# Optimization experiments

Hardware: AMD Instinct MI355X
Metric: run time of the kernel (lower is better)

The kernel has to match this reference:

```python
import jax, jax.numpy as jnp
import numpy as np

D_MODEL = 1024
HEADS = 16
HEAD_DIM = D_MODEL // HEADS
SEQ_LEN = 2048
BATCH = 2
LN_EPS = 1e-5


def _layernorm(x, gamma, beta):
    mu = jnp.mean(x, axis=-1, keepdims=True)
    var = jnp.var(x, axis=-1, keepdims=True)
    return (x - mu) * jax.lax.rsqrt(var + LN_EPS) * gamma + beta


def setup_inputs() -> dict:
    key = jax.random.key(0)
    ks = jax.random.split(key, 12)
    d, h = D_MODEL, 4 * D_MODEL
    s = lambda fan_in: 1.0 / np.sqrt(fan_in)
    return {
        "x": jax.random.normal(ks[0], (BATCH, SEQ_LEN, d), dtype=jnp.float32),
        "W_qkv": jax.random.uniform(ks[1], (d, 3 * d), minval=-s(d), maxval=s(d)),
        "b_qkv": jax.random.uniform(ks[2], (3 * d,), minval=-s(d), maxval=s(d)),
        "W1": jax.random.uniform(ks[3], (d, h), minval=-s(d), maxval=s(d)),
        "b1": jax.random.uniform(ks[4], (h,), minval=-s(d), maxval=s(d)),
        "W2": jax.random.uniform(ks[5], (h, d), minval=-s(h), maxval=s(h)),
        "b2": jax.random.uniform(ks[6], (d,), minval=-s(h), maxval=s(h)),
        "ln1_g": jnp.ones((d,), jnp.float32),
        "ln1_b": jnp.zeros((d,), jnp.float32),
        "ln2_g": jnp.ones((d,), jnp.float32),
        "ln2_b": jnp.zeros((d,), jnp.float32),
    }


def reference(x, W_qkv, b_qkv, W1, b1, W2, b2, ln1_g, ln1_b, ln2_g, ln2_b):
    B, T, C = x.shape
    # QKV projection -> [B, T, 3, H, hs] -> q,k,v each [B, H, T, hs]
    qkv = (x @ W_qkv + b_qkv).reshape(B, T, 3, HEADS, HEAD_DIM)
    qkv = jnp.transpose(qkv, (2, 0, 3, 1, 4))
    q, k, v = qkv[0], qkv[1], qkv[2]
    # Naive causal attention with full [B,H,T,T] score matrix (matches source)
    A = jnp.einsum("bhqd,bhkd->bhqk", q, k) / jnp.sqrt(jnp.float32(HEAD_DIM))
    causal = jnp.tril(jnp.ones((T, T), dtype=bool))
    A = jnp.where(causal, A, -jnp.inf)
    A = jax.nn.softmax(A, axis=-1)
    attn = jnp.einsum("bhqk,bhkd->bhqd", A, v)  # [B,H,T,hs]
    attn = jnp.transpose(attn, (0, 2, 1, 3)).reshape(B, T, C)
    # Residual + LN, FFN, residual + LN (dropout=0 / eval)
    h = _layernorm(x + attn, ln1_g, ln1_b)
    ff = jax.nn.relu(h @ W1 + b1) @ W2 + b2
    return _layernorm(h + ff, ln2_g, ln2_b)
```

## Files before the change

kernel.cpp:

```cpp
#include <hip/hip_runtime.h>

#define D_MODEL 1024
#define HEADS   16
#define HEAD_DIM 64
#define SEQ     2048
#define BATCH   2
#define ROWS    (BATCH*SEQ)
#define FFDIM   4096

typedef __attribute__((ext_vector_type(8))) short short8;
typedef __attribute__((ext_vector_type(4))) float f32x4;
typedef __attribute__((ext_vector_type(4))) unsigned short us4;

typedef const __attribute__((address_space(1))) unsigned int* gptr_t;
typedef __attribute__((address_space(3))) unsigned int* lptr_t;

__device__ __forceinline__ unsigned short f2bf(float f){
  unsigned int x = __float_as_uint(f);
  x += 0x7fffu + ((x >> 16) & 1u);
  return (unsigned short)(x >> 16);
}

__device__ __forceinline__ float wave_sum(float x){
  #pragma unroll
  for (int off = 32; off; off >>= 1) x += __shfl_xor(x, off);
  return x;
}

__global__ __launch_bounds__(256) void cast_bf16_kernel(const float* __restrict__ in,
                                                        unsigned short* __restrict__ out, int n4){
  int i = blockIdx.x * 256 + threadIdx.x;
  if (i >= n4) return;
  float4 v = *(const float4*)(in + (size_t)i * 4);
  us4 o;
  o[0] = f2bf(v.x); o[1] = f2bf(v.y); o[2] = f2bf(v.z); o[3] = f2bf(v.w);
  *(us4*)(out + (size_t)i * 4) = o;
}

__global__ __launch_bounds__(256) void transpose_cast_kernel(const float* __restrict__ in,
                                                             unsigned short* __restrict__ out,
                                                             int R, int C){
  __shared__ float tile[32][33];
  const int bc = blockIdx.x * 32, br = blockIdx.y * 32;
  const int tx = threadIdx.x & 31, ty = threadIdx.x >> 5;
  #pragma unroll
  for (int j = 0; j < 4; ++j)
    tile[ty + 8*j][tx] = in[(size_t)(br + ty + 8*j) * C + bc + tx];
  __syncthreads();
  #pragma unroll
  for (int j = 0; j < 4; ++j)
    out[(size_t)(bc + ty + 8*j) * R + br + tx] = f2bf(tile[tx][ty + 8*j]);
}

template<int EPI>
__global__ __launch_bounds__(512, 1) void gemm8p_kernel(const unsigned short* __restrict__ A,
                                                        const unsigned short* __restrict__ BT,
                                                        const float* __restrict__ bias,
                                                        int M, int N, int K, int kchunk,
                                                        int gx, int gy,
                                                        unsigned short* __restrict__ outH,
                                                        unsigned short* __restrict__ qo,
                                                        unsigned short* __restrict__ ko,
                                                        unsigned short* __restrict__ vT){
  __shared__ __align__(16) unsigned short Ab[2][2][256 * 32];
  __shared__ __align__(16) unsigned short Bb[2][2][256 * 32];
  const int tid = threadIdx.x, lane = tid & 63, wid = tid >> 6;
  const int wm = wid >> 2, wn = wid & 3;
  const int lr = lane & 15, g = lane >> 4;

  const int nwg = gridDim.x, cpx = nwg >> 3;
  const int wg = (blockIdx.x & 7) * cpx + (blockIdx.x >> 3);
  const int nx = wg % gx;
  const int rest = wg / gx;
  const int my = rest % gy;
  const int sk = rest / gy;
  const int m0 = my * 256, n0 = nx * 256, kb0 = sk * kchunk;
  const int nk = kchunk >> 6;

  f32x4 acc[8][4];
  #pragma unroll
  for (int i = 0; i < 8; ++i)
    #pragma unroll
    for (int j = 0; j < 4; ++j)
      acc[i][j] = f32x4{0.f, 0.f, 0.f, 0.f};

  auto STAGE = [&](int op, int t, int kh){
    const int d = t & 1;
    unsigned short* base = op ? &Bb[d][kh][0] : &Ab[d][kh][0];
    const unsigned short* src = op ? BT : A;
    const int r0 = op ? n0 : m0;
    #pragma unroll
    for (int j = 0; j < 2; ++j){
      const int L = tid + j * 512;
      const int row = L >> 2, c = L & 3;
      __builtin_amdgcn_global_load_lds(
          (gptr_t)(const void*)(src + (size_t)(r0 + row) * K + kb0 + t * 64 + kh * 32
                                + ((c ^ ((row >> 1) & 3)) << 3)),
          (lptr_t)(void*)(base + L * 8), 16, 0, 0);
    }
  };

  STAGE(0,0,0); STAGE(1,0,0); STAGE(0,0,1); STAGE(1,0,1);
  STAGE(0,1,0); STAGE(1,1,0); STAGE(0,1,1); STAGE(1,1,1);
  asm volatile("s_waitcnt vmcnt(8)" ::: "memory");
  __builtin_amdgcn_s_barrier();

  short8 afr[8], bfr[4];

  #define PHASE_SYNC(T)                                              \
    if ((T) < 2)              asm volatile("s_waitcnt vmcnt(4)" ::: "memory"); \
    else if ((T) <= nk - 3)   asm volatile("s_waitcnt vmcnt(8)" ::: "memory"); \
    else                      asm volatile("s_waitcnt vmcnt(0)" ::: "memory"); \
    __builtin_amdgcn_s_barrier();                                    \
    asm volatile("s_waitcnt lgkmcnt(0)" ::: "memory");               \
    __builtin_amdgcn_sched_barrier(0);

  for (int t = 0; t < nk; ++t){
    const int d = t & 1;
    #pragma unroll
    for (int i = 0; i < 8; ++i){
      const int row = wm * 128 + i * 16 + lr;
      afr[i] = *(const short8*)&Ab[d][0][row * 32 + ((g ^ ((row >> 1) & 3)) << 3)];
    }
    #pragma unroll
    for (int j = 0; j < 2; ++j){
      const int row = wn * 64 + j * 16 + lr;
      bfr[j] = *(const short8*)&Bb[d][0][row * 32 + ((g ^ ((row >> 1) & 3)) << 3)];
    }
    if (t >= 1 && t + 1 < nk) STAGE(1, t + 1, 1);
    PHASE_SYNC(t)
    __builtin_amdgcn_s_setprio(1);
    #pragma unroll
    for (int i = 0; i < 8; ++i){
      acc[i][0] = __builtin_amdgcn_mfma_f32_16x16x32_bf16(afr[i], bfr[0], acc[i][0], 0, 0, 0);
      acc[i][1] = __builtin_amdgcn_mfma_f32_16x16x32_bf16(afr[i], bfr[1], acc[i][1], 0, 0, 0);
    }
    __builtin_amdgcn_s_setprio(0);
    __builtin_amdgcn_s_barrier();

    #pragma unroll
    for (int j = 0; j < 2; ++j){
      const int row = wn * 64 + (2 + j) * 16 + lr;
      bfr[2 + j] = *(const short8*)&Bb[d][0][row * 32 + ((g ^ ((row >> 1) & 3)) << 3)];
    }
    if (t + 2 < nk) STAGE(0, t + 2, 0);
    PHASE_SYNC(t)
    __builtin_amdgcn_s_setprio(1);
    #pragma unroll
    for (int i = 0; i < 8; ++i){
      acc[i][2] = __builtin_amdgcn_mfma_f32_16x16x32_bf16(afr[i], bfr[2], acc[i][2], 0, 0, 0);
      acc[i][3] = __builtin_amdgcn_mfma_f32_16x16x32_bf16(afr[i], bfr[3], acc[i][3], 0, 0, 0);
    }
    __builtin_amdgcn_s_setprio(0);
    __builtin_amdgcn_s_barrier();

    #pragma unroll
    for (int i = 0; i < 8; ++i){
      const int row = wm * 128 + i * 16 + lr;
      afr[i] = *(const short8*)&Ab[d][1][row * 32 + ((g ^ ((row >> 1) & 3)) << 3)];
    }
    #pragma unroll
    for (int j = 0; j < 2; ++j){
      const int row = wn * 64 + j * 16 + lr;
      bfr[j] = *(const short8*)&Bb[d][1][row * 32 + ((g ^ ((row >> 1) & 3)) << 3)];
    }
    if (t + 2 < nk) STAGE(1, t + 2, 0);
    PHASE_SYNC(t)
    __builtin_amdgcn_s_setprio(1);
    #pragma unroll
    for (int i = 0; i < 8; ++i){
      acc[i][0] = __builtin_amdgcn_mfma_f32_16x16x32_bf16(afr[i], bfr[0], acc[i][0], 0, 0, 0);
      acc[i][1] = __builtin_amdgcn_mfma_f32_16x16x32_bf16(afr[i], bfr[1], acc[i][1], 0, 0, 0);
    }
    __builtin_amdgcn_s_setprio(0);
    __builtin_amdgcn_s_barrier();

    #pragma unroll
    for (int j = 0; j < 2; ++j){
      const int row = wn * 64 + (2 + j) * 16 + lr;
      bfr[2 + j] = *(const short8*)&Bb[d][1][row * 32 + ((g ^ ((row >> 1) & 3)) << 3)];
    }
    if (t + 2 < nk) STAGE(0, t + 2, 1);
    PHASE_SYNC(t)
    __builtin_amdgcn_s_setprio(1);
    #pragma unroll
    for (int i = 0; i < 8; ++i){
      acc[i][2] = __builtin_amdgcn_mfma_f32_16x16x32_bf16(afr[i], bfr[2], acc[i][2], 0, 0, 0);
      acc[i][3] = __builtin_amdgcn_mfma_f32_16x16x32_bf16(afr[i], bfr[3], acc[i][3], 0, 0, 0);
    }
    __builtin_amdgcn_s_setprio(0);
    __builtin_amdgcn_s_barrier();
  }
  #undef PHASE_SYNC

  #pragma unroll
  for (int i = 0; i < 8; ++i){
    const int rg = m0 + wm * 128 + i * 16 + g * 4;
    #pragma unroll
    for (int j = 0; j < 4; ++j){
      const int cg = n0 + wn * 64 + j * 16 + lr;
      if constexpr (EPI == 0){
        const float bb = bias[cg];
        const int which = cg >> 10, rem = cg & 1023;
        const int hh = rem >> 6, dd = rem & 63;
        const int bb_ = rg >> 11, tt = rg & 2047;
        const size_t bh = (size_t)(bb_ * HEADS + hh);
        if (which == 2){
          us4 pk;
          #pragma unroll
          for (int r = 0; r < 4; ++r) pk[r] = f2bf(acc[i][j][r] + bb);
          *(us4*)(vT + (bh * 64 + dd) * SEQ + tt) = pk;
        } else {
          unsigned short* dst = which ? ko : qo;
          const float sc2 = which ? 1.0f : 0.18033688f;
          #pragma unroll
          for (int r = 0; r < 4; ++r)
            dst[(bh * SEQ + tt + r) * 64 + dd] = f2bf((acc[i][j][r] + bb) * sc2);
        }
      } else if constexpr (EPI == 1){
        const float bb = bias[cg];
        #pragma unroll
        for (int r = 0; r < 4; ++r)
          outH[(size_t)(rg + r) * N + cg] = f2bf(fmaxf(acc[i][j][r] + bb, 0.f));
      } else {
        unsigned short* dst = outH + (size_t)sk * M * N;
        #pragma unroll
        for (int r = 0; r < 4; ++r)
          dst[(size_t)(rg + r) * N + cg] = f2bf(acc[i][j][r]);
      }
    }
  }
}

template<int EPI>
__global__ __launch_bounds__(256) void gemm_kernel(const unsigned short* __restrict__ A,
                                                   const unsigned short* __restrict__ BT,
                                                   const float* __restrict__ bias,
                                                   int M, int N, int K, int kchunk,
                                                   int gx, int gy,
                                                   float* __restrict__ outF,
                                                   unsigned short* __restrict__ outH){
  __shared__ __align__(16) unsigned short Alds[2][128 * 32];
  __shared__ __align__(16) unsigned short Blds[2][128 * 32];
  const int tid = threadIdx.x;
  const int lane = tid & 63;
  const int wid = tid >> 6;
  const int wr = wid >> 1, wc = wid & 1;
  const int lrow = lane & 15, lgrp = lane >> 4;

  const int nwg = gridDim.x;
  const int cpx = nwg >> 3;
  const int wg = (blockIdx.x & 7) * cpx + (blockIdx.x >> 3);
  const int nx = wg % gx;
  const int rest = wg / gx;
  const int my = rest % gy;
  const int sk = rest / gy;

  const int m0 = my * 128, n0 = nx * 128;
  const int kbase0 = sk * kchunk;
  const int sr = lane >> 2, sc = (lane & 3) * 8;

  f32x4 acc[4][4];
  #pragma unroll
  for (int i = 0; i < 4; ++i)
    #pragma unroll
    for (int j = 0; j < 4; ++j)
      acc[i][j] = f32x4{0.f, 0.f, 0.f, 0.f};

  #pragma unroll
  for (int it = 0; it < 2; ++it){
    const int c = wid * 2 + it;
    const int r = c * 16 + sr;
    __builtin_amdgcn_global_load_lds(
        (gptr_t)(const void*)(A + (size_t)(m0 + r) * K + kbase0 + sc),
        (lptr_t)(void*)(&Alds[0][c * 512]), 16, 0, 0);
    __builtin_amdgcn_global_load_lds(
        (gptr_t)(const void*)(BT + (size_t)(n0 + r) * K + kbase0 + sc),
        (lptr_t)(void*)(&Blds[0][c * 512]), 16, 0, 0);
  }

  const int nk = kchunk >> 5;
  int cur = 0;
  for (int kt = 0; kt < nk; ++kt){
    __syncthreads();
    if (kt + 1 < nk){
      const int kb = kbase0 + (kt + 1) * 32;
      #pragma unroll
      for (int it = 0; it < 2; ++it){
        const int c = wid * 2 + it;
        const int r = c * 16 + sr;
        __builtin_amdgcn_global_load_lds(
            (gptr_t)(const void*)(A + (size_t)(m0 + r) * K + kb + sc),
            (lptr_t)(void*)(&Alds[cur ^ 1][c * 512]), 16, 0, 0);
        __builtin_amdgcn_global_load_lds(
            (gptr_t)(const void*)(BT + (size_t)(n0 + r) * K + kb + sc),
            (lptr_t)(void*)(&Blds[cur ^ 1][c * 512]), 16, 0, 0);
      }
    }
    short8 af[4], bfr[4];
    #pragma unroll
    for (int f = 0; f < 4; ++f){
      af[f]  = *(const short8*)&Alds[cur][(wr * 64 + f * 16 + lrow) * 32 + lgrp * 8];
      bfr[f] = *(const short8*)&Blds[cur][(wc * 64 + f * 16 + lrow) * 32 + lgrp * 8];
    }
    #pragma unroll
    for (int i = 0; i < 4; ++i)
      #pragma unroll
      for (int j = 0; j < 4; ++j)
        acc[i][j] = __builtin_amdgcn_mfma_f32_16x16x32_bf16(af[i], bfr[j], acc[i][j], 0, 0, 0);
    cur ^= 1;
  }

  float* const outP = outF + (size_t)sk * M * N;
  #pragma unroll
  for (int i = 0; i < 4; ++i){
    const int rg = m0 + wr * 64 + i * 16 + lgrp * 4;
    #pragma unroll
    for (int j = 0; j < 4; ++j){
      const int cg = n0 + wc * 64 + j * 16 + lrow;
      #pragma unroll
      for (int r = 0; r < 4; ++r)
        outP[(size_t)(rg + r) * N + cg] = acc[i][j][r];
    }
  }
  (void)bias; (void)outH;
}

__global__ __launch_bounds__(256) void attn_mfma_kernel(const unsigned short* __restrict__ Qb,
                                                        const unsigned short* __restrict__ Kb,
                                                        const unsigned short* __restrict__ VT,
                                                        float* __restrict__ Op){
  __shared__ __align__(16) char Kl[2][8192];
  __shared__ __align__(16) char Vl[2][8192];
  __shared__ __align__(16) char Pl[4][4096];
  const int tid = threadIdx.x;
  const int w = tid >> 6, lane = tid & 63;
  const int lr = lane & 15, g = lane >> 4;

  const int bx = blockIdx.x, u = bx & 255, half = bx >> 8;
  const int g8 = u >> 5;
  const int qg = half ? g8 : 15 - g8;
  const int bh = u & 31;

  const int q0w = qg * 128 + w * 32;
  const int qA = q0w + lr, qB = qA + 16;

  const char* const KbB = (const char*)(Kb + (size_t)bh * SEQ * 64);
  const char* const VbB = (const char*)(VT + (size_t)bh * 64 * SEQ);
  char* const PbA = Pl[w];
  char* const PbB = Pl[w] + 2048;

  const unsigned short* qra = Qb + ((size_t)bh * SEQ + qA) * 64 + g * 8;
  const short8 qfA0 = *(const short8*)(qra);
  const short8 qfA1 = *(const short8*)(qra + 32);
  const short8 qfB0 = *(const short8*)(qra + 16 * 64);
  const short8 qfB1 = *(const short8*)(qra + 16 * 64 + 32);

  f32x4 oA[4], oB[4];
  #pragma unroll
  for (int dt = 0; dt < 4; ++dt){ oA[dt] = f32x4{0.f,0.f,0.f,0.f}; oB[dt] = f32x4{0.f,0.f,0.f,0.f}; }
  float lA = 0.f, lB = 0.f;
  const int swzl = (lr & 7) << 4;

  const int kbmax = 2 * qg + 1;

  short8 st[4];
  {
    #pragma unroll
    for (int c = 0; c < 2; ++c){
      const int L = c * 4096 + tid * 16;
      st[c] = *(const short8*)(KbB + L);
      const int row = L >> 7, col = L & 127;
      st[2 + c] = *(const short8*)(VbB + (size_t)row * 4096 + col);
    }
  }

  for (int kb = 0; kb <= kbmax; ++kb){
    const int p = kb & 1;
    const int k0 = kb * 64;

    #pragma unroll
    for (int c = 0; c < 2; ++c){
      const int L = c * 4096 + tid * 16;
      const int row = L >> 7, col = L & 127;
      const int dst = row * 128 + (col ^ ((row & 7) << 4));
      *(short8*)(Kl[p] + dst) = st[c];
      *(short8*)(Vl[p] + dst) = st[2 + c];
    }
    __syncthreads();

    if (kb < kbmax){
      #pragma unroll
      for (int c = 0; c < 2; ++c){
        const int L = c * 4096 + tid * 16;
        st[c] = *(const short8*)(KbB + (size_t)(kb + 1) * 8192 + L);
        const int row = L >> 7, col = L & 127;
        st[2 + c] = *(const short8*)(VbB + (size_t)row * 4096 + (size_t)(kb + 1) * 128 + col);
      }
    }

    f32x4 sA[4], sB[4];
    __builtin_amdgcn_s_setprio(1);
    #pragma unroll
    for (int kt = 0; kt < 4; ++kt){
      const int row = kt * 16 + lr;
      const int ro = row * 128, sw = (row & 7) << 4;
      const short8 kf0 = *(const short8*)(Kl[p] + ro + ((g * 16) ^ sw));
      const short8 kf1 = *(const short8*)(Kl[p] + ro + ((64 + g * 16) ^ sw));
      sA[kt] = __builtin_amdgcn_mfma_f32_16x16x32_bf16(kf0, qfA0, f32x4{0.f,0.f,0.f,0.f}, 0, 0, 0);
      sA[kt] = __builtin_amdgcn_mfma_f32_16x16x32_bf16(kf1, qfA1, sA[kt], 0, 0, 0);
      sB[kt] = __builtin_amdgcn_mfma_f32_16x16x32_bf16(kf0, qfB0, f32x4{0.f,0.f,0.f,0.f}, 0, 0, 0);
      sB[kt] = __builtin_amdgcn_mfma_f32_16x16x32_bf16(kf1, qfB1, sB[kt], 0, 0, 0);
    }
    __builtin_amdgcn_s_setprio(0);

    if (kb >= kbmax - 1){
      #pragma unroll
      for (int kt = 0; kt < 4; ++kt)
        #pragma unroll
        for (int r = 0; r < 4; ++r){
          const int key = k0 + kt * 16 + g * 4 + r;
          if (key > qA) sA[kt][r] = -INFINITY;
          if (key > qB) sB[kt][r] = -INFINITY;
        }
    }

    {
      float sum = 0.f;
      #pragma unroll
      for (int kt = 0; kt < 4; ++kt){
        #pragma unroll
        for (int r = 0; r < 4; ++r){
          const float pp = __builtin_amdgcn_exp2f(sA[kt][r]);
          sA[kt][r] = pp; sum += pp;
        }
        unsigned int p01, p23;
        asm("v_cvt_pk_bf16_f32 %0, %1, %2" : "=v"(p01) : "v"(sA[kt][0]), "v"(sA[kt][1]));
        asm("v_cvt_pk_bf16_f32 %0, %1, %2" : "=v"(p23) : "v"(sA[kt][2]), "v"(sA[kt][3]));
        uint2 pk; pk.x = p01; pk.y = p23;
        *(uint2*)(PbA + lr * 128 + ((kt * 32 + g * 8) ^ swzl)) = pk;
      }
      sum += __shfl_xor(sum, 16);
      sum += __shfl_xor(sum, 32);
      lA += sum;
    }
    {
      float sum = 0.f;
      #pragma unroll
      for (int kt = 0; kt < 4; ++kt){
        #pragma unroll
        for (int r = 0; r < 4; ++r){
          const float pp = __builtin_amdgcn_exp2f(sB[kt][r]);
          sB[kt][r] = pp; sum += pp;
        }
        unsigned int p01, p23;
        asm("v_cvt_pk_bf16_f32 %0, %1, %2" : "=v"(p01) : "v"(sB[kt][0]), "v"(sB[kt][1]));
        asm("v_cvt_pk_bf16_f32 %0, %1, %2" : "=v"(p23) : "v"(sB[kt][2]), "v"(sB[kt][3]));
        uint2 pk; pk.x = p01; pk.y = p23;
        *(uint2*)(PbB + lr * 128 + ((kt * 32 + g * 8) ^ swzl)) = pk;
      }
      sum += __shfl_xor(sum, 16);
      sum += __shfl_xor(sum, 32);
      lB += sum;
    }

    const short8 paA0 = *(const short8*)(PbA + lr * 128 + ((g * 16) ^ swzl));
    const short8 paA1 = *(const short8*)(PbA + lr * 128 + ((64 + g * 16) ^ swzl));
    const short8 paB0 = *(const short8*)(PbB + lr * 128 + ((g * 16) ^ swzl));
    const short8 paB1 = *(const short8*)(PbB + lr * 128 + ((64 + g * 16) ^ swzl));
    __builtin_amdgcn_s_setprio(1);
    #pragma unroll
    for (int dt = 0; dt < 4; ++dt){
      const int row = dt * 16 + lr;
      const int ro = row * 128, sw = (row & 7) << 4;
      const short8 vf0 = *(const short8*)(Vl[p] + ro + ((g * 16) ^ sw));
      const short8 vf1 = *(const short8*)(Vl[p] + ro + ((64 + g * 16) ^ sw));
      oA[dt] = __builtin_amdgcn_mfma_f32_16x16x32_bf16(paA0, vf0, oA[dt], 0, 0, 0);
      oA[dt] = __builtin_amdgcn_mfma_f32_16x16x32_bf16(paA1, vf1, oA[dt], 0, 0, 0);
      oB[dt] = __builtin_amdgcn_mfma_f32_16x16x32_bf16(paB0, vf0, oB[dt], 0, 0, 0);
      oB[dt] = __builtin_amdgcn_mfma_f32_16x16x32_bf16(paB1, vf1, oB[dt], 0, 0, 0);
    }
    __builtin_amdgcn_s_setprio(0);
  }

  const int b = bh >> 4, hh = bh & 15;
  {
    float lv[4];
    #pragma unroll
    for (int r = 0; r < 4; ++r) lv[r] = __shfl(lA, g * 4 + r);
    #pragma unroll
    for (int dt = 0; dt < 4; ++dt)
      #pragma unroll
      for (int r = 0; r < 4; ++r)
        Op[((size_t)(b * SEQ) + q0w + g * 4 + r) * D_MODEL + hh * 64 + dt * 16 + lr] = oA[dt][r] / lv[r];
  }
  {
    float lv[4];
    #pragma unroll
    for (int r = 0; r < 4; ++r) lv[r] = __shfl(lB, g * 4 + r);
    #pragma unroll
    for (int dt = 0; dt < 4; ++dt)
      #pragma unroll
      for (int r = 0; r < 4; ++r)
        Op[((size_t)(b * SEQ) + q0w + 16 + g * 4 + r) * D_MODEL + hh * 64 + dt * 16 + lr] = oB[dt][r] / lv[r];
  }
}

__global__ __launch_bounds__(256) void ln_kernel(const float* __restrict__ A,
                                                 const float* __restrict__ B1,
                                                 const unsigned short* __restrict__ P4,
                                                 size_t pstride,
                                                 const float* __restrict__ bias,
                                                 const float* __restrict__ g,
                                                 const float* __restrict__ be,
                                                 float* __restrict__ outF,
                                                 unsigned short* __restrict__ outH){
  const int row = blockIdx.x, tid = threadIdx.x;
  const size_t base = (size_t)row * D_MODEL + tid * 4;
  float4 va = *(const float4*)(A + base);
  float v0 = va.x, v1 = va.y, v2 = va.z, v3 = va.w;
  if (B1){
    float4 vb = *(const float4*)(B1 + base);
    v0 += vb.x; v1 += vb.y; v2 += vb.z; v3 += vb.w;
  }
  if (P4){
    #pragma unroll
    for (int p = 0; p < 4; ++p){
      us4 u = *(const us4*)(P4 + p * pstride + base);
      v0 += __uint_as_float((unsigned int)u[0] << 16);
      v1 += __uint_as_float((unsigned int)u[1] << 16);
      v2 += __uint_as_float((unsigned int)u[2] << 16);
      v3 += __uint_as_float((unsigned int)u[3] << 16);
    }
  }
  if (bias){
    float4 vd = *(const float4*)(bias + tid * 4);
    v0 += vd.x; v1 += vd.y; v2 += vd.z; v3 += vd.w;
  }
  float s  = v0 + v1 + v2 + v3;
  float ss = v0*v0 + v1*v1 + v2*v2 + v3*v3;
  s = wave_sum(s); ss = wave_sum(ss);
  __shared__ float red[8];
  const int w = tid >> 6, lane = tid & 63;
  if (!lane){ red[w] = s; red[4 + w] = ss; }
  __syncthreads();
  s  = red[0] + red[1] + red[2] + red[3];
  ss = red[4] + red[5] + red[6] + red[7];
  const float mu  = s * (1.0f / D_MODEL);
  const float var = ss * (1.0f / D_MODEL) - mu * mu;
  const float rstd = rsqrtf(var + 1e-5f);
  float4 gg = *(const float4*)(g  + tid * 4);
  float4 bb = *(const float4*)(be + tid * 4);
  const float r0 = (v0 - mu) * rstd * gg.x + bb.x;
  const float r1 = (v1 - mu) * rstd * gg.y + bb.y;
  const float r2 = (v2 - mu) * rstd * gg.z + bb.z;
  const float r3 = (v3 - mu) * rstd * gg.w + bb.w;
  float4 of; of.x = r0; of.y = r1; of.z = r2; of.w = r3;
  *(float4*)(outF + base) = of;
  if (outH){
    us4 oh; oh[0] = f2bf(r0); oh[1] = f2bf(r1); oh[2] = f2bf(r2); oh[3] = f2bf(r3);
    *(us4*)(outH + base) = oh;
  }
}

__global__ __launch_bounds__(256) void ln2f_kernel(const float* __restrict__ A,
                                                   const float* __restrict__ B1,
                                                   const float* __restrict__ bias,
                                                   const float* __restrict__ g,
                                                   const float* __restrict__ be,
                                                   float* __restrict__ outF){
  const int row = blockIdx.x, tid = threadIdx.x;
  const size_t base = (size_t)row * D_MODEL + tid * 4;
  float4 va = *(const float4*)(A + base);
  float4 vb = *(const float4*)(B1 + base);
  float4 vd = *(const float4*)(bias + tid * 4);
  float v0 = va.x + vb.x + vd.x, v1 = va.y + vb.y + vd.y;
  float v2 = va.z + vb.z + vd.z, v3 = va.w + vb.w + vd.w;
  float s  = v0 + v1 + v2 + v3;
  float ss = v0*v0 + v1*v1 + v2*v2 + v3*v3;
  s = wave_sum(s); ss = wave_sum(ss);
  __shared__ float red[8];
  const int w = tid >> 6, lane = tid & 63;
  if (!lane){ red[w] = s; red[4 + w] = ss; }
  __syncthreads();
  s  = red[0] + red[1] + red[2] + red[3];
  ss = red[4] + red[5] + red[6] + red[7];
  const float mu  = s * (1.0f / D_MODEL);
  const float var = ss * (1.0f / D_MODEL) - mu * mu;
  const float rstd = rsqrtf(var + 1e-5f);
  float4 gg = *(const float4*)(g  + tid * 4);
  float4 bb = *(const float4*)(be + tid * 4);
  float4 of;
  of.x = (v0 - mu) * rstd * gg.x + bb.x;
  of.y = (v1 - mu) * rstd * gg.y + bb.y;
  of.z = (v2 - mu) * rstd * gg.z + bb.z;
  of.w = (v3 - mu) * rstd * gg.w + bb.w;
  *(float4*)(outF + base) = of;
}

extern "C" void kernel_launch(void* const* d_in, const int* in_sizes, int n_in,
                              void* d_out, int out_size, void* d_ws, size_t ws_size,
                              hipStream_t stream){
  (void)in_sizes; (void)n_in; (void)out_size;
  const float* x     = (const float*)d_in[0];
  const float* W_qkv = (const float*)d_in[1];
  const float* b_qkv = (const float*)d_in[2];
  const float* W1    = (const float*)d_in[3];
  const float* b1    = (const float*)d_in[4];
  const float* W2    = (const float*)d_in[5];
  const float* b2    = (const float*)d_in[6];
  const float* ln1g  = (const float*)d_in[7];
  const float* ln1b  = (const float*)d_in[8];
  const float* ln2g  = (const float*)d_in[9];
  const float* ln2b  = (const float*)d_in[10];

  char* ws = (char*)d_ws;
  const size_t MB = 1024ull * 1024ull;
  unsigned short* WqkvT = (unsigned short*)(ws + 0 * MB);
  unsigned short* W1T   = (unsigned short*)(ws + 6 * MB);
  unsigned short* W2T   = (unsigned short*)(ws + 14 * MB);
  unsigned short* xbf   = (unsigned short*)(ws + 22 * MB);
  unsigned short* qB    = (unsigned short*)(ws + 30 * MB);
  unsigned short* kB    = (unsigned short*)(ws + 39 * MB);
  unsigned short* vT    = (unsigned short*)(ws + 48 * MB);
  float* attn = (float*)(ws + 57 * MB);
  float* hF           = (float*)(ws + 30 * MB);
  unsigned short* hB  = (unsigned short*)(ws + 46 * MB);
  unsigned short* ff1 = (unsigned short*)(ws + 54 * MB);
  unsigned short* pbf = (unsigned short*)(ws + 86 * MB);
  float* p0           = (float*)(ws + 86 * MB);

  const int use8p = (ws_size >= 118 * MB);

  cast_bf16_kernel<<<4096, 256, 0, stream>>>(x, xbf, ROWS * D_MODEL / 4);
  transpose_cast_kernel<<<dim3(96, 32), 256, 0, stream>>>(W_qkv, WqkvT, 1024, 3072);
  transpose_cast_kernel<<<dim3(128, 32), 256, 0, stream>>>(W1, W1T, 1024, 4096);
  transpose_cast_kernel<<<dim3(32, 128), 256, 0, stream>>>(W2, W2T, 4096, 1024);

  gemm8p_kernel<0><<<192, 512, 0, stream>>>(
      xbf, WqkvT, b_qkv, ROWS, 3072, 1024, 1024, 12, 16, nullptr, qB, kB, vT);

  attn_mfma_kernel<<<512, 256, 0, stream>>>(qB, kB, vT, attn);

  ln_kernel<<<ROWS, 256, 0, stream>>>(x, attn, nullptr, 0, nullptr, ln1g, ln1b, hF, hB);

  gemm8p_kernel<1><<<256, 512, 0, stream>>>(
      hB, W1T, b1, ROWS, FFDIM, 1024, 1024, 16, 16, ff1, nullptr, nullptr, nullptr);

  if (use8p){
    gemm8p_kernel<4><<<256, 512, 0, stream>>>(
        ff1, W2T, nullptr, ROWS, 1024, FFDIM, 1024, 4, 16, pbf, nullptr, nullptr, nullptr);
    ln_kernel<<<ROWS, 256, 0, stream>>>(hF, nullptr, pbf, (size_t)ROWS * 1024, b2,
                                        ln2g, ln2b, (float*)d_out, nullptr);
  } else {
    gemm_kernel<3><<<256, 256, 0, stream>>>(
        ff1, W2T, nullptr, ROWS, 1024, FFDIM, FFDIM, 8, 32, p0, nullptr);
    ln2f_kernel<<<ROWS, 256, 0, stream>>>(hF, p0, b2, ln2g, ln2b, (float*)d_out);
  }
}
```

Measured before the change: 206.2 us.

## Move QKV GEMM to 128-tile kernel and retune 8-phase vmcnt waits

The QKV projection now runs on the simpler 128x128 double-buffered GEMM with 768 workgroups instead of the 256x256 eight-phase kernel with 192 workgroups, which left most of the 256 CUs idle. The 8-phase kernel, still used for the FFN GEMMs, gets a different waitcnt scheme: the initial wait allows 12 loads in flight and waits happen only in two of the four phases, so more loads stay outstanding. The smaller-tile GEMM reuses less data per load and uses a simpler pipeline, and the looser waits need careful counting to stay correct.

```diff
diff --git a/kernel.cpp b/kernel.cpp
--- a/kernel.cpp
+++ b/kernel.cpp
@@ -53,152 +53,94 @@
 }
 
 template<int EPI>
-__global__ __launch_bounds__(512, 1) void gemm8p_kernel(const unsigned short* __restrict__ A,
-                                                        const unsigned short* __restrict__ BT,
-                                                        const float* __restrict__ bias,
-                                                        int M, int N, int K, int kchunk,
-                                                        int gx, int gy,
-                                                        unsigned short* __restrict__ outH,
-                                                        unsigned short* __restrict__ qo,
-                                                        unsigned short* __restrict__ ko,
-                                                        unsigned short* __restrict__ vT){
-  __shared__ __align__(16) unsigned short Ab[2][2][256 * 32];
-  __shared__ __align__(16) unsigned short Bb[2][2][256 * 32];
-  const int tid = threadIdx.x, lane = tid & 63, wid = tid >> 6;
-  const int wm = wid >> 2, wn = wid & 3;
-  const int lr = lane & 15, g = lane >> 4;
-
-  const int nwg = gridDim.x, cpx = nwg >> 3;
+__global__ __launch_bounds__(256) void gemm_kernel(const unsigned short* __restrict__ A,
+                                                   const unsigned short* __restrict__ BT,
+                                                   const float* __restrict__ bias,
+                                                   int M, int N, int K, int kchunk,
+                                                   int gx, int gy,
+                                                   float* __restrict__ outF,
+                                                   unsigned short* __restrict__ qo,
+                                                   unsigned short* __restrict__ ko,
+                                                   unsigned short* __restrict__ vT){
+  __shared__ __align__(16) unsigned short Alds[2][128 * 32];
+  __shared__ __align__(16) unsigned short Blds[2][128 * 32];
+  const int tid = threadIdx.x;
+  const int lane = tid & 63;
+  const int wid = tid >> 6;
+  const int wr = wid >> 1, wc = wid & 1;
+  const int lrow = lane & 15, lgrp = lane >> 4;
+
+  const int nwg = gridDim.x;
+  const int cpx = nwg >> 3;
   const int wg = (blockIdx.x & 7) * cpx + (blockIdx.x >> 3);
   const int nx = wg % gx;
   const int rest = wg / gx;
   const int my = rest % gy;
   const int sk = rest / gy;
-  const int m0 = my * 256, n0 = nx * 256, kb0 = sk * kchunk;
-  const int nk = kchunk >> 6;
-
-  f32x4 acc[8][4];
-  #pragma unroll
-  for (int i = 0; i < 8; ++i)
+
+  const int m0 = my * 128, n0 = nx * 128;
+  const int kbase0 = sk * kchunk;
+  const int sr = lane >> 2, sc = (lane & 3) * 8;
+
+  f32x4 acc[4][4];
+  #pragma unroll
+  for (int i = 0; i < 4; ++i)
     #pragma unroll
     for (int j = 0; j < 4; ++j)
       acc[i][j] = f32x4{0.f, 0.f, 0.f, 0.f};
 
-  auto STAGE = [&](int op, int t, int kh){
-    const int d = t & 1;
-    unsigned short* base = op ? &Bb[d][kh][0] : &Ab[d][kh][0];
-    const unsigned short* src = op ? BT : A;
-    const int r0 = op ? n0 : m0;
-    #pragma unroll
-    for (int j = 0; j < 2; ++j){
-      const int L = tid + j * 512;
-      const int row = L >> 2, c = L & 3;
-      __builtin_amdgcn_global_load_lds(
-          (gptr_t)(const void*)(src + (size_t)(r0 + row) * K + kb0 + t * 64 + kh * 32
-                                + ((c ^ ((row >> 1) & 3)) << 3)),
-          (lptr_t)(void*)(base + L * 8), 16, 0, 0);
-    }
-  };
-
-  STAGE(0,0,0); STAGE(1,0,0); STAGE(0,0,1); STAGE(1,0,1);
-  STAGE(0,1,0); STAGE(1,1,0); STAGE(0,1,1); STAGE(1,1,1);
-  asm volatile("s_waitcnt vmcnt(8)" ::: "memory");
-  __builtin_amdgcn_s_barrier();
-
-  short8 afr[8], bfr[4];
-
-  #define PHASE_SYNC(T)                                              \
-    if ((T) < 2)              asm volatile("s_waitcnt vmcnt(4)" ::: "memory"); \
-    else if ((T) <= nk - 3)   asm volatile("s_waitcnt vmcnt(8)" ::: "memory"); \
-    else                      asm volatile("s_waitcnt vmcnt(0)" ::: "memory"); \
-    __builtin_amdgcn_s_barrier();                                    \
-    asm volatile("s_waitcnt lgkmcnt(0)" ::: "memory");               \
-    __builtin_amdgcn_sched_barrier(0);
-
-  for (int t = 0; t < nk; ++t){
-    const int d = t & 1;
-    #pragma unroll
-    for (int i = 0; i < 8; ++i){
-      const int row = wm * 128 + i * 16 + lr;
-      afr[i] = *(const short8*)&Ab[d][0][row * 32 + ((g ^ ((row >> 1) & 3)) << 3)];
-    }
-    #pragma unroll
-    for (int j = 0; j < 2; ++j){
-      const int row = wn * 64 + j * 16 + lr;
-      bfr[j] = *(const short8*)&Bb[d][0][row * 32 + ((g ^ ((row >> 1) & 3)) << 3)];
-    }
-    if (t >= 1 && t + 1 < nk) STAGE(1, t + 1, 1);
-    PHASE_SYNC(t)
+  #pragma unroll
+  for (int it = 0; it < 2; ++it){
+    const int c = wid * 2 + it;
+    const int r = c * 16 + sr;
+    __builtin_amdgcn_global_load_lds(
+        (gptr_t)(const void*)(A + (size_t)(m0 + r) * K + kbase0 + sc),
+        (lptr_t)(void*)(&Alds[0][c * 512]), 16, 0, 0);
+    __builtin_amdgcn_global_load_lds(
+        (gptr_t)(const void*)(BT + (size_t)(n0 + r) * K + kbase0 + sc),
+        (lptr_t)(void*)(&Blds[0][c * 512]), 16, 0, 0);
+  }
+
+  const int nk = kchunk >> 5;
+  int cur = 0;
+  for (int kt = 0; kt < nk; ++kt){
+    __syncthreads();
+    if (kt + 1 < nk){
+      const int kb = kbase0 + (kt + 1) * 32;
+      #pragma unroll
+      for (int it = 0; it < 2; ++it){
+        const int c = wid * 2 + it;
+        const int r = c * 16 + sr;
+        __builtin_amdgcn_global_load_lds(
+            (gptr_t)(const void*)(A + (size_t)(m0 + r) * K + kb + sc),
+            (lptr_t)(void*)(&Alds[cur ^ 1][c * 512]), 16, 0, 0);
+        __builtin_amdgcn_global_load_lds(
+            (gptr_t)(const void*)(BT + (size_t)(n0 + r) * K + kb + sc),
+            (lptr_t)(void*)(&Blds[cur ^ 1][c * 512]), 16, 0, 0);
+      }
+    }
+    short8 af[4], bfr[4];
+    #pragma unroll
+    for (int f = 0; f < 4; ++f){
+      af[f]  = *(const short8*)&Alds[cur][(wr * 64 + f * 16 + lrow) * 32 + lgrp * 8];
+      bfr[f] = *(const short8*)&Blds[cur][(wc * 64 + f * 16 + lrow) * 32 + lgrp * 8];
+    }
     __builtin_amdgcn_s_setprio(1);
     #pragma unroll
-    for (int i = 0; i < 8; ++i){
-      acc[i][0] = __builtin_amdgcn_mfma_f32_16x16x32_bf16(afr[i], bfr[0], acc[i][0], 0, 0, 0);
-      acc[i][1] = __builtin_amdgcn_mfma_f32_16x16x32_bf16(afr[i], bfr[1], acc[i][1], 0, 0, 0);
-    }
+    for (int i = 0; i < 4; ++i)
+      #pragma unroll
+      for (int j = 0; j < 4; ++j)
+        acc[i][j] = __builtin_amdgcn_mfma_f32_16x16x32_bf16(af[i], bfr[j], acc[i][j], 0, 0, 0);
     __builtin_amdgcn_s_setprio(0);
-    __builtin_amdgcn_s_barrier();
-
-    #pragma unroll
-    for (int j = 0; j < 2; ++j){
-      const int row = wn * 64 + (2 + j) * 16 + lr;
-      bfr[2 + j] = *(const short8*)&Bb[d][0][row * 32 + ((g ^ ((row >> 1) & 3)) << 3)];
-    }
-    if (t + 2 < nk) STAGE(0, t + 2, 0);
-    PHASE_SYNC(t)
-    __builtin_amdgcn_s_setprio(1);
-    #pragma unroll
-    for (int i = 0; i < 8; ++i){
-      acc[i][2] = __builtin_amdgcn_mfma_f32_16x16x32_bf16(afr[i], bfr[2], acc[i][2], 0, 0, 0);
-      acc[i][3] = __builtin_amdgcn_mfma_f32_16x16x32_bf16(afr[i], bfr[3], acc[i][3], 0, 0, 0);
-    }
-    __builtin_amdgcn_s_setprio(0);
-    __builtin_amdgcn_s_barrier();
-
-    #pragma unroll
-    for (int i = 0; i < 8; ++i){
-      const int row = wm * 128 + i * 16 + lr;
-      afr[i] = *(const short8*)&Ab[d][1][row * 32 + ((g ^ ((row >> 1) & 3)) << 3)];
-    }
-    #pragma unroll
-    for (int j = 0; j < 2; ++j){
-      const int row = wn * 64 + j * 16 + lr;
-      bfr[j] = *(const short8*)&Bb[d][1][row * 32 + ((g ^ ((row >> 1) & 3)) << 3)];
-    }
-    if (t + 2 < nk) STAGE(1, t + 2, 0);
-    PHASE_SYNC(t)
-    __builtin_amdgcn_s_setprio(1);
-    #pragma unroll
-    for (int i = 0; i < 8; ++i){
-      acc[i][0] = __builtin_amdgcn_mfma_f32_16x16x32_bf16(afr[i], bfr[0], acc[i][0], 0, 0, 0);
-      acc[i][1] = __builtin_amdgcn_mfma_f32_16x16x32_bf16(afr[i], bfr[1], acc[i][1], 0, 0, 0);
-    }
-    __builtin_amdgcn_s_setprio(0);
-    __builtin_amdgcn_s_barrier();
-
-    #pragma unroll
-    for (int j = 0; j < 2; ++j){
-      const int row = wn * 64 + (2 + j) * 16 + lr;
-      bfr[2 + j] = *(const short8*)&Bb[d][1][row * 32 + ((g ^ ((row >> 1) & 3)) << 3)];
-    }
-    if (t + 2 < nk) STAGE(0, t + 2, 1);
-    PHASE_SYNC(t)
-    __builtin_amdgcn_s_setprio(1);
-    #pragma unroll
-    for (int i = 0; i < 8; ++i){
-      acc[i][2] = __builtin_amdgcn_mfma_f32_16x16x32_bf16(afr[i], bfr[2], acc[i][2], 0, 0, 0);
-      acc[i][3] = __builtin_amdgcn_mfma_f32_16x16x32_bf16(afr[i], bfr[3], acc[i][3], 0, 0, 0);
-    }
-    __builtin_amdgcn_s_setprio(0);
-    __builtin_amdgcn_s_barrier();
-  }
-  #undef PHASE_SYNC
-
-  #pragma unroll
-  for (int i = 0; i < 8; ++i){
-    const int rg = m0 + wm * 128 + i * 16 + g * 4;
+    cur ^= 1;
+  }
+
+  #pragma unroll
+  for (int i = 0; i < 4; ++i){
+    const int rg = m0 + wr * 64 + i * 16 + lgrp * 4;
     #pragma unroll
     for (int j = 0; j < 4; ++j){
-      const int cg = n0 + wn * 64 + j * 16 + lr;
+      const int cg = n0 + wc * 64 + j * 16 + lrow;
       if constexpr (EPI == 0){
         const float bb = bias[cg];
         const int which = cg >> 10, rem = cg & 1023;
@@ -217,7 +159,163 @@
           for (int r = 0; r < 4; ++r)
             dst[(bh * SEQ + tt + r) * 64 + dd] = f2bf((acc[i][j][r] + bb) * sc2);
         }
-      } else if constexpr (EPI == 1){
+      } else {
+        float* outP = outF + (size_t)sk * M * N;
+        #pragma unroll
+        for (int r = 0; r < 4; ++r)
+          outP[(size_t)(rg + r) * N + cg] = acc[i][j][r];
+      }
+    }
+  }
+}
+
+template<int EPI>
+__global__ __launch_bounds__(512, 1) void gemm8p_kernel(const unsigned short* __restrict__ A,
+                                                        const unsigned short* __restrict__ BT,
+                                                        const float* __restrict__ bias,
+                                                        int M, int N, int K, int kchunk,
+                                                        int gx, int gy,
+                                                        unsigned short* __restrict__ outH){
+  __shared__ __align__(16) unsigned short Ab[2][2][256 * 32];
+  __shared__ __align__(16) unsigned short Bb[2][2][256 * 32];
+  const int tid = threadIdx.x, lane = tid & 63, wid = tid >> 6;
+  const int wm = wid >> 2, wn = wid & 3;
+  const int lr = lane & 15, g = lane >> 4;
+
+  const int nwg = gridDim.x, cpx = nwg >> 3;
+  const int wg = (blockIdx.x & 7) * cpx + (blockIdx.x >> 3);
+  const int nx = wg % gx;
+  const int rest = wg / gx;
+  const int my = rest % gy;
+  const int sk = rest / gy;
+  const int m0 = my * 256, n0 = nx * 256, kb0 = sk * kchunk;
+  const int nk = kchunk >> 6;
+
+  f32x4 acc[8][4];
+  #pragma unroll
+  for (int i = 0; i < 8; ++i)
+    #pragma unroll
+    for (int j = 0; j < 4; ++j)
+      acc[i][j] = f32x4{0.f, 0.f, 0.f, 0.f};
+
+  auto STAGE = [&](int op, int t, int kh){
+    const int d = t & 1;
+    unsigned short* base = op ? &Bb[d][kh][0] : &Ab[d][kh][0];
+    const unsigned short* src = op ? BT : A;
+    const int r0 = op ? n0 : m0;
+    #pragma unroll
+    for (int j = 0; j < 2; ++j){
+      const int L = tid + j * 512;
+      const int row = L >> 2, c = L & 3;
+      __builtin_amdgcn_global_load_lds(
+          (gptr_t)(const void*)(src + (size_t)(r0 + row) * K + kb0 + t * 64 + kh * 32
+                                + ((c ^ ((row >> 1) & 3)) << 3)),
+          (lptr_t)(void*)(base + L * 8), 16, 0, 0);
+    }
+  };
+
+  STAGE(0,0,0); STAGE(1,0,0); STAGE(0,0,1); STAGE(1,0,1);
+  STAGE(0,1,0); STAGE(1,1,0); STAGE(0,1,1); STAGE(1,1,1);
+  asm volatile("s_waitcnt vmcnt(12)" ::: "memory");
+  __builtin_amdgcn_s_barrier();
+
+  short8 afr[8], bfr[4];
+
+  #define SYNC_NOV()                                              \
+    __builtin_amdgcn_s_barrier();                                 \
+    asm volatile("s_waitcnt lgkmcnt(0)" ::: "memory");            \
+    __builtin_amdgcn_sched_barrier(0);
+
+  for (int t = 0; t < nk; ++t){
+    const int d = t & 1;
+    #pragma unroll
+    for (int i = 0; i < 8; ++i){
+      const int row = wm * 128 + i * 16 + lr;
+      afr[i] = *(const short8*)&Ab[d][0][row * 32 + ((g ^ ((row >> 1) & 3)) << 3)];
+    }
+    #pragma unroll
+    for (int j = 0; j < 2; ++j){
+      const int row = wn * 64 + j * 16 + lr;
+      bfr[j] = *(const short8*)&Bb[d][0][row * 32 + ((g ^ ((row >> 1) & 3)) << 3)];
+    }
+    if (t >= 1 && t + 1 < nk) STAGE(1, t + 1, 1);
+    SYNC_NOV()
+    __builtin_amdgcn_s_setprio(1);
+    #pragma unroll
+    for (int i = 0; i < 8; ++i){
+      acc[i][0] = __builtin_amdgcn_mfma_f32_16x16x32_bf16(afr[i], bfr[0], acc[i][0], 0, 0, 0);
+      acc[i][1] = __builtin_amdgcn_mfma_f32_16x16x32_bf16(afr[i], bfr[1], acc[i][1], 0, 0, 0);
+    }
+    __builtin_amdgcn_s_setprio(0);
+    __builtin_amdgcn_s_barrier();
+
+    #pragma unroll
+    for (int j = 0; j < 2; ++j){
+      const int row = wn * 64 + (2 + j) * 16 + lr;
+      bfr[2 + j] = *(const short8*)&Bb[d][0][row * 32 + ((g ^ ((row >> 1) & 3)) << 3)];
+    }
+    if (t + 2 < nk) STAGE(0, t + 2, 0);
+    if (t + 2 < nk)      asm volatile("s_waitcnt vmcnt(10)" ::: "memory");
+    else if (t + 1 < nk) asm volatile("s_waitcnt vmcnt(8)"  ::: "memory");
+    else                 asm volatile("s_waitcnt vmcnt(0)"  ::: "memory");
+    SYNC_NOV()
+    __builtin_amdgcn_s_setprio(1);
+    #pragma unroll
+    for (int i = 0; i < 8; ++i){
+      acc[i][2] = __builtin_amdgcn_mfma_f32_16x16x32_bf16(afr[i], bfr[2], acc[i][2], 0, 0, 0);
+      acc[i][3] = __builtin_amdgcn_mfma_f32_16x16x32_bf16(afr[i], bfr[3], acc[i][3], 0, 0, 0);
+    }
+    __builtin_amdgcn_s_setprio(0);
+    __builtin_amdgcn_s_barrier();
+
+    #pragma unroll
+    for (int i = 0; i < 8; ++i){
+      const int row = wm * 128 + i * 16 + lr;
+      afr[i] = *(const short8*)&Ab[d][1][row * 32 + ((g ^ ((row >> 1) & 3)) << 3)];
+    }
+    #pragma unroll
+    for (int j = 0; j < 2; ++j){
+      const int row = wn * 64 + j * 16 + lr;
+      bfr[j] = *(const short8*)&Bb[d][1][row * 32 + ((g ^ ((row >> 1) & 3)) << 3)];
+    }
+    if (t + 2 < nk) STAGE(1, t + 2, 0);
+    SYNC_NOV()
+    __builtin_amdgcn_s_setprio(1);
+    #pragma unroll
+    for (int i = 0; i < 8; ++i){
+      acc[i][0] = __builtin_amdgcn_mfma_f32_16x16x32_bf16(afr[i], bfr[0], acc[i][0], 0, 0, 0);
+      acc[i][1] = __builtin_amdgcn_mfma_f32_16x16x32_bf16(afr[i], bfr[1], acc[i][1], 0, 0, 0);
+    }
+    __builtin_amdgcn_s_setprio(0);
+    __builtin_amdgcn_s_barrier();
+
+    #pragma unroll
+    for (int j = 0; j < 2; ++j){
+      const int row = wn * 64 + (2 + j) * 16 + lr;
+      bfr[2 + j] = *(const short8*)&Bb[d][1][row * 32 + ((g ^ ((row >> 1) & 3)) << 3)];
+    }
+    if (t + 2 < nk) STAGE(0, t + 2, 1);
+    if (t + 2 < nk)      asm volatile("s_waitcnt vmcnt(10)" ::: "memory");
+    else if (t + 1 < nk) asm volatile("s_waitcnt vmcnt(4)"  ::: "memory");
+    SYNC_NOV()
+    __builtin_amdgcn_s_setprio(1);
+    #pragma unroll
+    for (int i = 0; i < 8; ++i){
+      acc[i][2] = __builtin_amdgcn_mfma_f32_16x16x32_bf16(afr[i], bfr[2], acc[i][2], 0, 0, 0);
+      acc[i][3] = __builtin_amdgcn_mfma_f32_16x16x32_bf16(afr[i], bfr[3], acc[i][3], 0, 0, 0);
+    }
+    __builtin_amdgcn_s_setprio(0);
+    __builtin_amdgcn_s_barrier();
+  }
+  #undef SYNC_NOV
+
+  #pragma unroll
+  for (int i = 0; i < 8; ++i){
+    const int rg = m0 + wm * 128 + i * 16 + g * 4;
+    #pragma unroll
+    for (int j = 0; j < 4; ++j){
+      const int cg = n0 + wn * 64 + j * 16 + lr;
+      if constexpr (EPI == 1){
         const float bb = bias[cg];
         #pragma unroll
         for (int r = 0; r < 4; ++r)
@@ -230,100 +328,6 @@
       }
     }
   }
-}
-
-template<int EPI>
-__global__ __launch_bounds__(256) void gemm_kernel(const unsigned short* __restrict__ A,
-                                                   const unsigned short* __restrict__ BT,
-                                                   const float* __restrict__ bias,
-                                                   int M, int N, int K, int kchunk,
-                                                   int gx, int gy,
-                                                   float* __restrict__ outF,
-                                                   unsigned short* __restrict__ outH){
-  __shared__ __align__(16) unsigned short Alds[2][128 * 32];
-  __shared__ __align__(16) unsigned short Blds[2][128 * 32];
-  const int tid = threadIdx.x;
-  const int lane = tid & 63;
-  const int wid = tid >> 6;
-  const int wr = wid >> 1, wc = wid & 1;
-  const int lrow = lane & 15, lgrp = lane >> 4;
-
-  const int nwg = gridDim.x;
-  const int cpx = nwg >> 3;
-  const int wg = (blockIdx.x & 7) * cpx + (blockIdx.x >> 3);
-  const int nx = wg % gx;
-  const int rest = wg / gx;
-  const int my = rest % gy;
-  const int sk = rest / gy;
-
-  const int m0 = my * 128, n0 = nx * 128;
-  const int kbase0 = sk * kchunk;
-  const int sr = lane >> 2, sc = (lane & 3) * 8;
-
-  f32x4 acc[4][4];
-  #pragma unroll
-  for (int i = 0; i < 4; ++i)
-    #pragma unroll
-    for (int j = 0; j < 4; ++j)
-      acc[i][j] = f32x4{0.f, 0.f, 0.f, 0.f};
-
-  #pragma unroll
-  for (int it = 0; it < 2; ++it){
-    const int c = wid * 2 + it;
-    const int r = c * 16 + sr;
-    __builtin_amdgcn_global_load_lds(
-        (gptr_t)(const void*)(A + (size_t)(m0 + r) * K + kbase0 + sc),
-        (lptr_t)(void*)(&Alds[0][c * 512]), 16, 0, 0);
-    __builtin_amdgcn_global_load_lds(
-        (gptr_t)(const void*)(BT + (size_t)(n0 + r) * K + kbase0 + sc),
-        (lptr_t)(void*)(&Blds[0][c * 512]), 16, 0, 0);
-  }
-
-  const int nk = kchunk >> 5;
-  int cur = 0;
-  for (int kt = 0; kt < nk; ++kt){
-    __syncthreads();
-    if (kt + 1 < nk){
-      const int kb = kbase0 + (kt + 1) * 32;
-      #pragma unroll
-      for (int it = 0; it < 2; ++it){
-        const int c = wid * 2 + it;
-        const int r = c * 16 + sr;
-        __builtin_amdgcn_global_load_lds(
-            (gptr_t)(const void*)(A + (size_t)(m0 + r) * K + kb + sc),
-            (lptr_t)(void*)(&Alds[cur ^ 1][c * 512]), 16, 0, 0);
-        __builtin_amdgcn_global_load_lds(
-            (gptr_t)(const void*)(BT + (size_t)(n0 + r) * K + kb + sc),
-            (lptr_t)(void*)(&Blds[cur ^ 1][c * 512]), 16, 0, 0);
-      }
-    }
-    short8 af[4], bfr[4];
-    #pragma unroll
-    for (int f = 0; f < 4; ++f){
-      af[f]  = *(const short8*)&Alds[cur][(wr * 64 + f * 16 + lrow) * 32 + lgrp * 8];
-      bfr[f] = *(const short8*)&Blds[cur][(wc * 64 + f * 16 + lrow) * 32 + lgrp * 8];
-    }
-    #pragma unroll
-    for (int i = 0; i < 4; ++i)
-      #pragma unroll
-      for (int j = 0; j < 4; ++j)
-        acc[i][j] = __builtin_amdgcn_mfma_f32_16x16x32_bf16(af[i], bfr[j], acc[i][j], 0, 0, 0);
-    cur ^= 1;
-  }
-
-  float* const outP = outF + (size_t)sk * M * N;
-  #pragma unroll
-  for (int i = 0; i < 4; ++i){
-    const int rg = m0 + wr * 64 + i * 16 + lgrp * 4;
-    #pragma unroll
-    for (int j = 0; j < 4; ++j){
-      const int cg = n0 + wc * 64 + j * 16 + lrow;
-      #pragma unroll
-      for (int r = 0; r < 4; ++r)
-        outP[(size_t)(rg + r) * N + cg] = acc[i][j][r];
-    }
-  }
-  (void)bias; (void)outH;
 }
 
 __global__ __launch_bounds__(256) void attn_mfma_kernel(const unsigned short* __restrict__ Qb,
@@ -637,24 +641,24 @@
   transpose_cast_kernel<<<dim3(128, 32), 256, 0, stream>>>(W1, W1T, 1024, 4096);
   transpose_cast_kernel<<<dim3(32, 128), 256, 0, stream>>>(W2, W2T, 4096, 1024);
 
-  gemm8p_kernel<0><<<192, 512, 0, stream>>>(
-      xbf, WqkvT, b_qkv, ROWS, 3072, 1024, 1024, 12, 16, nullptr, qB, kB, vT);
+  gemm_kernel<0><<<768, 256, 0, stream>>>(
+      xbf, WqkvT, b_qkv, ROWS, 3072, 1024, 1024, 24, 32, nullptr, qB, kB, vT);
 
   attn_mfma_kernel<<<512, 256, 0, stream>>>(qB, kB, vT, attn);
 
   ln_kernel<<<ROWS, 256, 0, stream>>>(x, attn, nullptr, 0, nullptr, ln1g, ln1b, hF, hB);
 
   gemm8p_kernel<1><<<256, 512, 0, stream>>>(
-      hB, W1T, b1, ROWS, FFDIM, 1024, 1024, 16, 16, ff1, nullptr, nullptr, nullptr);
+      hB, W1T, b1, ROWS, FFDIM, 1024, 1024, 16, 16, ff1);
 
   if (use8p){
     gemm8p_kernel<4><<<256, 512, 0, stream>>>(
-        ff1, W2T, nullptr, ROWS, 1024, FFDIM, 1024, 4, 16, pbf, nullptr, nullptr, nullptr);
+        ff1, W2T, nullptr, ROWS, 1024, FFDIM, 1024, 4, 16, pbf);
     ln_kernel<<<ROWS, 256, 0, stream>>>(hF, nullptr, pbf, (size_t)ROWS * 1024, b2,
                                         ln2g, ln2b, (float*)d_out, nullptr);
   } else {
     gemm_kernel<3><<<256, 256, 0, stream>>>(
-        ff1, W2T, nullptr, ROWS, 1024, FFDIM, FFDIM, 8, 32, p0, nullptr);
+        ff1, W2T, nullptr, ROWS, 1024, FFDIM, FFDIM, 8, 32, p0, nullptr, nullptr, nullptr);
     ln2f_kernel<<<ROWS, 256, 0, stream>>>(hF, p0, b2, ln2g, ln2b, (float*)d_out);
   }
 }
```

After: 200.5 us. -2.7%, faster.
